# Performance work log

Measured on AMD Instinct MI355X. Metric: run time of the kernel, lower is better.

The kernel has to match this reference:

```python
import jax, jax.numpy as jnp
import numpy as np

EPS = 1e-06
NUM_HEADS = 8


def phi(x):
    # elu(x) + 1, a positive feature map
    return jax.nn.elu(x) + 1.0


def setup_inputs() -> dict:
    key = jax.random.key(0)
    ks = jax.random.split(key, 7)
    B, N, E = 4, 1024, 512
    s = 1.0 / np.sqrt(E)
    return {
        "Q": jax.random.normal(ks[0], (B, N, E), jnp.float32),
        "K": jax.random.normal(ks[1], (B, N, E), jnp.float32),
        "V": jax.random.normal(ks[2], (B, N, E), jnp.float32),
        "Wq": jax.random.normal(ks[3], (E, E), jnp.float32) * s,
        "Wk": jax.random.normal(ks[4], (E, E), jnp.float32) * s,
        "Wv": jax.random.normal(ks[5], (E, E), jnp.float32) * s,
        "Wo": jax.random.normal(ks[6], (E, E), jnp.float32) * s,
        "causal": 1,
    }


def _split_heads(x, H):
    B, N, E = x.shape
    return x.reshape(B, N, H, E // H).transpose(0, 2, 1, 3)  # (B,H,N,D)


def reference(Q, K, V, Wq, Wk, Wv, Wo, causal):
    B, N, E = Q.shape
    H = NUM_HEADS
    D = E // H
    # nn.Linear: y = x @ W.T (bias=False)
    Qf = phi(_split_heads(Q @ Wq.T, H))  # (B,H,N,D)
    Kf = phi(_split_heads(K @ Wk.T, H))  # (B,H,N,D)
    Vh = _split_heads(V @ Wv.T, H)       # (B,H,N,D)

    if causal:
        # prefix sums of outer products K_f V^T -> (B,H,N,D,Dv)
        KV_prefix = jnp.cumsum(Kf[..., :, None] * Vh[..., None, :], axis=2)
        Kf_prefix = jnp.cumsum(Kf, axis=2)
        num = jnp.einsum('bhnd,bhnde->bhne', Qf, KV_prefix)
        den = jnp.einsum('bhnd,bhnd->bhn', Qf, Kf_prefix)[..., None]
        out = num / (den + EPS)
    else:
        KV = jnp.einsum('bhnd,bhne->bhde', Kf, Vh)          # (B,H,D,Dv)
        Kf_sum = Kf.sum(axis=2)                              # (B,H,D)
        num = jnp.einsum('bhnd,bhde->bhne', Qf, KV)
        den = jnp.einsum('bhnd,bhd->bhn', Qf, Kf_sum)[..., None]
        out = num / (den + EPS)

    out = out.transpose(0, 2, 1, 3).reshape(B, N, E)
    return out @ Wo.T
```

## Files before the change

### kernel.cpp

```cpp
#include <hip/hip_runtime.h>
#include <stdint.h>

typedef __bf16 bf16;
typedef __attribute__((ext_vector_type(8))) __bf16 bfx8;
typedef __attribute__((ext_vector_type(4))) float f32x4;

__device__ inline f32x4 mfma16(bfx8 a, bfx8 b, f32x4 c) {
  return __builtin_amdgcn_mfma_f32_16x16x32_bf16(a, b, c, 0, 0, 0);
}

struct GemmArgs {
  const void* A[3];
  const void* Bt[3];
  bf16* ob[3];
  float* of;
  int phi_upto;
};

template <bool AF32, bool BF32, bool OUTF>
__global__ __launch_bounds__(256) void gemm_bt(GemmArgs ga) {
  const int z = blockIdx.z;
  const void* Ag = ga.A[z];
  const void* Bg = ga.Bt[z];
  const int tm = blockIdx.x * 128, tn = blockIdx.y * 128;
  const int tid = threadIdx.x, l = tid & 63, w = tid >> 6;
  const int wm = w >> 1, wn = w & 1, lm = l & 15, lk = l >> 4;

  __shared__ __align__(16) bf16 As[128 * 64];
  __shared__ __align__(16) bf16 Bs[128 * 64];

  f32x4 acc[4][4] = {};

  for (int kt = 0; kt < 8; ++kt) {
#pragma unroll
    for (int it = 0; it < 4; ++it) {
      int c = (it * 4 + w) * 64 + l;
      int row = c >> 3, t8 = c & 7;
      bfx8 v;
      if (AF32) {
        const float* s = (const float*)Ag + (size_t)(tm + row) * 512 + kt * 64 + t8 * 8;
        f32x4 x0 = *(const f32x4*)s;
        f32x4 x1 = *(const f32x4*)(s + 4);
        v[0] = (bf16)x0[0]; v[1] = (bf16)x0[1]; v[2] = (bf16)x0[2]; v[3] = (bf16)x0[3];
        v[4] = (bf16)x1[0]; v[5] = (bf16)x1[1]; v[6] = (bf16)x1[2]; v[7] = (bf16)x1[3];
      } else {
        v = *(const bfx8*)((const bf16*)Ag + (size_t)(tm + row) * 512 + kt * 64 + t8 * 8);
      }
      *(bfx8*)&As[row * 64 + ((t8 ^ (row & 7)) << 3)] = v;
    }
#pragma unroll
    for (int it = 0; it < 4; ++it) {
      int c = (it * 4 + w) * 64 + l;
      int row = c >> 3, t8 = c & 7;
      bfx8 v;
      if (BF32) {
        const float* s = (const float*)Bg + (size_t)(tn + row) * 512 + kt * 64 + t8 * 8;
        f32x4 x0 = *(const f32x4*)s;
        f32x4 x1 = *(const f32x4*)(s + 4);
        v[0] = (bf16)x0[0]; v[1] = (bf16)x0[1]; v[2] = (bf16)x0[2]; v[3] = (bf16)x0[3];
        v[4] = (bf16)x1[0]; v[5] = (bf16)x1[1]; v[6] = (bf16)x1[2]; v[7] = (bf16)x1[3];
      } else {
        v = *(const bfx8*)((const bf16*)Bg + (size_t)(tn + row) * 512 + kt * 64 + t8 * 8);
      }
      *(bfx8*)&Bs[row * 64 + ((t8 ^ (row & 7)) << 3)] = v;
    }
    __syncthreads();
#pragma unroll
    for (int ks = 0; ks < 2; ++ks) {
      bfx8 af[4], bfr[4];
#pragma unroll
      for (int i = 0; i < 4; ++i) {
        int ra = wm * 64 + i * 16 + lm;
        af[i] = *(const bfx8*)&As[ra * 64 + (((ks * 4 + lk) ^ (ra & 7)) << 3)];
        int rb = wn * 64 + i * 16 + lm;
        bfr[i] = *(const bfx8*)&Bs[rb * 64 + (((ks * 4 + lk) ^ (rb & 7)) << 3)];
      }
#pragma unroll
      for (int i = 0; i < 4; ++i)
#pragma unroll
        for (int j = 0; j < 4; ++j)
          acc[i][j] = mfma16(af[i], bfr[j], acc[i][j]);
    }
    __syncthreads();
  }

  const bool phi = z < ga.phi_upto;
#pragma unroll
  for (int i = 0; i < 4; ++i)
#pragma unroll
    for (int j = 0; j < 4; ++j)
#pragma unroll
      for (int r = 0; r < 4; ++r) {
        int m = tm + wm * 64 + i * 16 + lk * 4 + r;
        int n = tn + wn * 64 + j * 16 + lm;
        float v = acc[i][j][r];
        if (phi) v = v > 0.f ? v + 1.f : __expf(v);
        if (OUTF) ga.of[(size_t)m * 512 + n] = v;
        else ga.ob[z][(size_t)m * 512 + n] = (bf16)v;
      }
}

__global__ __launch_bounds__(256) void chunk_kv(const bf16* __restrict__ Kf,
                                                const bf16* __restrict__ Vh,
                                                float* __restrict__ KVs,
                                                float* __restrict__ ksums) {
  const int bh = blockIdx.x, c = blockIdx.y, b = bh >> 3, h = bh & 7;
  const int tid = threadIdx.x, l = tid & 63, w = tid >> 6, lm = l & 15, lk = l >> 4;
  __shared__ __align__(16) bf16 KTs[64 * 64];
  __shared__ __align__(16) bf16 VTs[64 * 64];
  __shared__ float ksum_p[256];

  const size_t base = (size_t)(b * 1024) * 512 + h * 64;
  const int sr = tid >> 2, sp = tid & 3;
  {
    const size_t g = base + (size_t)(c * 64 + sr) * 512 + sp * 16;
    bfx8 k0 = *(const bfx8*)&Kf[g], k1 = *(const bfx8*)&Kf[g + 8];
    bfx8 v0 = *(const bfx8*)&Vh[g], v1 = *(const bfx8*)&Vh[g + 8];
#pragma unroll
    for (int q = 0; q < 8; ++q) {
      int d0 = sp * 16 + q, d1 = sp * 16 + 8 + q;
      KTs[d0 * 64 + (((sr >> 3) ^ (d0 & 7)) << 3) + (sr & 7)] = k0[q];
      KTs[d1 * 64 + (((sr >> 3) ^ (d1 & 7)) << 3) + (sr & 7)] = k1[q];
      VTs[d0 * 64 + (((sr >> 3) ^ (d0 & 7)) << 3) + (sr & 7)] = v0[q];
      VTs[d1 * 64 + (((sr >> 3) ^ (d1 & 7)) << 3) + (sr & 7)] = v1[q];
    }
  }
  __syncthreads();
  {
    int d = tid & 63, jp = tid >> 6;
    float s = 0.f;
#pragma unroll
    for (int q = 0; q < 16; ++q) {
      int j = jp * 16 + q;
      s += (float)KTs[d * 64 + (((j >> 3) ^ (d & 7)) << 3) + (j & 7)];
    }
    ksum_p[jp * 64 + d] = s;
  }
  f32x4 kacc[4] = {};
#pragma unroll
  for (int ks = 0; ks < 2; ++ks) {
    int r = w * 16 + lm;
    bfx8 av = *(const bfx8*)&VTs[r * 64 + (((ks * 4 + lk) ^ (r & 7)) << 3)];
#pragma unroll
    for (int bn = 0; bn < 4; ++bn) {
      int e = bn * 16 + lm;
      bfx8 bk = *(const bfx8*)&KTs[e * 64 + (((ks * 4 + lk) ^ (e & 7)) << 3)];
      kacc[bn] = mfma16(av, bk, kacc[bn]);
    }
  }
  float* st = KVs + (size_t)(bh * 16 + c) * 4096;
#pragma unroll
  for (int bn = 0; bn < 4; ++bn)
#pragma unroll
    for (int rg = 0; rg < 4; ++rg) {
      int e = w * 16 + lk * 4 + rg, d = bn * 16 + lm;
      st[e * 64 + d] = kacc[bn][rg];
    }
  __syncthreads();
  if (tid < 64)
    ksums[(size_t)(bh * 16 + c) * 64 + tid] =
        ksum_p[tid] + ksum_p[64 + tid] + ksum_p[128 + tid] + ksum_p[192 + tid];
}

__global__ __launch_bounds__(256) void scan_kv(float* __restrict__ KVs,
                                               float* __restrict__ ksums) {
  const int bh = blockIdx.x, slice = blockIdx.y;
  const int tid = threadIdx.x;
  float* p = KVs + (size_t)bh * 16 * 4096 + slice * 256 + tid;
  float run = 0.f;
#pragma unroll
  for (int c = 0; c < 16; ++c) {
    float t = p[(size_t)c * 4096];
    p[(size_t)c * 4096] = run;
    run += t;
  }
  if (slice == 0 && tid < 64) {
    float* kp = ksums + (size_t)bh * 16 * 64 + tid;
    float rk = 0.f;
#pragma unroll
    for (int c = 0; c < 16; ++c) {
      float t = kp[(size_t)c * 64];
      kp[(size_t)c * 64] = rk;
      rk += t;
    }
  }
}

__global__ __launch_bounds__(256) void chunk_out(const bf16* __restrict__ Qf,
                                                 const bf16* __restrict__ Kf,
                                                 const bf16* __restrict__ Vh,
                                                 const float* __restrict__ KVs,
                                                 const float* __restrict__ ksums,
                                                 bf16* __restrict__ Ob) {
  const int bh = blockIdx.x, c = blockIdx.y, b = bh >> 3, h = bh & 7;
  const int tid = threadIdx.x, l = tid & 63, w = tid >> 6, lm = l & 15, lk = l >> 4;

  __shared__ __align__(16) bf16 Qs[64 * 64];
  __shared__ __align__(16) bf16 Ks[64 * 64];
  __shared__ __align__(16) bf16 VTs[64 * 64];
  __shared__ __align__(16) bf16 Ss[64 * 64];
  __shared__ float ksum[64], den_i[64], den_all[64], den_p[256];

  const size_t base = (size_t)(b * 1024) * 512 + h * 64;
  const int sr = tid >> 2, sp = tid & 3;
  {
    const size_t g = base + (size_t)(c * 64 + sr) * 512 + sp * 16;
    bfx8 q0 = *(const bfx8*)&Qf[g], q1 = *(const bfx8*)&Qf[g + 8];
    bfx8 k0 = *(const bfx8*)&Kf[g], k1 = *(const bfx8*)&Kf[g + 8];
    bfx8 v0 = *(const bfx8*)&Vh[g], v1 = *(const bfx8*)&Vh[g + 8];
    *(bfx8*)&Qs[sr * 64 + (((2 * sp) ^ (sr & 7)) << 3)] = q0;
    *(bfx8*)&Qs[sr * 64 + (((2 * sp + 1) ^ (sr & 7)) << 3)] = q1;
    *(bfx8*)&Ks[sr * 64 + (((2 * sp) ^ (sr & 7)) << 3)] = k0;
    *(bfx8*)&Ks[sr * 64 + (((2 * sp + 1) ^ (sr & 7)) << 3)] = k1;
#pragma unroll
    for (int q = 0; q < 8; ++q) {
      int d0 = sp * 16 + q, d1 = sp * 16 + 8 + q;
      VTs[d0 * 64 + (((sr >> 3) ^ (d0 & 7)) << 3) + (sr & 7)] = v0[q];
      VTs[d1 * 64 + (((sr >> 3) ^ (d1 & 7)) << 3) + (sr & 7)] = v1[q];
    }
  }
  if (tid < 64) ksum[tid] = ksums[(size_t)(bh * 16 + c) * 64 + tid];
  __syncthreads();

  f32x4 sacc[4] = {};
  bfx8 aq[2];
#pragma unroll
  for (int ks = 0; ks < 2; ++ks) {
    int r = w * 16 + lm;
    aq[ks] = *(const bfx8*)&Qs[r * 64 + (((ks * 4 + lk) ^ (r & 7)) << 3)];
#pragma unroll
    for (int bn = 0; bn < 4; ++bn) {
      int rb = bn * 16 + lm;
      bfx8 bk = *(const bfx8*)&Ks[rb * 64 + (((ks * 4 + lk) ^ (rb & 7)) << 3)];
      sacc[bn] = mfma16(aq[ks], bk, sacc[bn]);
    }
  }
  float prs[4] = {0.f, 0.f, 0.f, 0.f};
#pragma unroll
  for (int bn = 0; bn < 4; ++bn)
#pragma unroll
    for (int rg = 0; rg < 4; ++rg) {
      int i = w * 16 + lk * 4 + rg, j = bn * 16 + lm;
      float v = (j <= i) ? sacc[bn][rg] : 0.f;
      prs[rg] += v;
      Ss[i * 64 + (((j >> 3) ^ (i & 7)) << 3) + (j & 7)] = (bf16)v;
    }
#pragma unroll
  for (int m = 1; m < 16; m <<= 1) {
#pragma unroll
    for (int rg = 0; rg < 4; ++rg) prs[rg] += __shfl_xor(prs[rg], m, 64);
  }
  if (lm == 0) {
#pragma unroll
    for (int rg = 0; rg < 4; ++rg) den_i[w * 16 + lk * 4 + rg] = prs[rg];
  }
  {
    float s = 0.f;
#pragma unroll
    for (int q = 0; q < 16; ++q) {
      int d = sp * 16 + q;
      s += (float)Qs[sr * 64 + (((d >> 3) ^ (sr & 7)) << 3) + (d & 7)] * ksum[d];
    }
    den_p[sp * 64 + sr] = s;
  }
  __syncthreads();

  if (tid < 64)
    den_all[tid] = den_i[tid] + den_p[tid] + den_p[64 + tid] + den_p[128 + tid] + den_p[192 + tid];
  f32x4 oacc[4] = {};
  const float* st = KVs + (size_t)(bh * 16 + c) * 4096;
#pragma unroll
  for (int ks = 0; ks < 2; ++ks) {
    int r = w * 16 + lm;
    bfx8 as_ = *(const bfx8*)&Ss[r * 64 + (((ks * 4 + lk) ^ (r & 7)) << 3)];
#pragma unroll
    for (int bn = 0; bn < 4; ++bn) {
      int e = bn * 16 + lm;
      bfx8 bv = *(const bfx8*)&VTs[e * 64 + (((ks * 4 + lk) ^ (e & 7)) << 3)];
      oacc[bn] = mfma16(as_, bv, oacc[bn]);
      int d0 = ks * 32 + lk * 8;
      f32x4 x0 = *(const f32x4*)&st[e * 64 + d0];
      f32x4 x1 = *(const f32x4*)&st[e * 64 + d0 + 4];
      bfx8 bkv;
      bkv[0] = (bf16)x0[0]; bkv[1] = (bf16)x0[1]; bkv[2] = (bf16)x0[2]; bkv[3] = (bf16)x0[3];
      bkv[4] = (bf16)x1[0]; bkv[5] = (bf16)x1[1]; bkv[6] = (bf16)x1[2]; bkv[7] = (bf16)x1[3];
      oacc[bn] = mfma16(aq[ks], bkv, oacc[bn]);
    }
  }
  __syncthreads();

#pragma unroll
  for (int bn = 0; bn < 4; ++bn)
#pragma unroll
    for (int rg = 0; rg < 4; ++rg) {
      int i = w * 16 + lk * 4 + rg, e = bn * 16 + lm;
      float o = oacc[bn][rg] / (den_all[i] + 1e-6f);
      Ob[base + (size_t)(c * 64 + i) * 512 + e] = (bf16)o;
    }
}

extern "C" void kernel_launch(void* const* d_in, const int* in_sizes, int n_in,
                              void* d_out, int out_size, void* d_ws, size_t ws_size,
                              hipStream_t stream) {
  const float* Q = (const float*)d_in[0];
  const float* K = (const float*)d_in[1];
  const float* V = (const float*)d_in[2];
  const float* Wq = (const float*)d_in[3];
  const float* Wk = (const float*)d_in[4];
  const float* Wv = (const float*)d_in[5];
  const float* Wo = (const float*)d_in[6];
  (void)in_sizes; (void)n_in; (void)out_size; (void)ws_size;

  char* wsp = (char*)d_ws;
  const size_t MB = 1ull << 20;
  bf16* Qp = (bf16*)(wsp + 0 * MB);
  bf16* Kp = (bf16*)(wsp + 4 * MB);
  bf16* Vp = (bf16*)(wsp + 8 * MB);
  bf16* Ob = (bf16*)(wsp + 12 * MB);
  float* KVs = (float*)(wsp + 16 * MB);
  float* ksums = (float*)(wsp + 24 * MB);

  GemmArgs g1;
  g1.A[0] = Q;  g1.A[1] = K;  g1.A[2] = V;
  g1.Bt[0] = Wq; g1.Bt[1] = Wk; g1.Bt[2] = Wv;
  g1.ob[0] = Qp; g1.ob[1] = Kp; g1.ob[2] = Vp;
  g1.of = nullptr;
  g1.phi_upto = 2;
  gemm_bt<true, true, false><<<dim3(32, 4, 3), 256, 0, stream>>>(g1);

  chunk_kv<<<dim3(32, 16), 256, 0, stream>>>(Kp, Vp, KVs, ksums);
  scan_kv<<<dim3(32, 16), 256, 0, stream>>>(KVs, ksums);
  chunk_out<<<dim3(32, 16), 256, 0, stream>>>(Qp, Kp, Vp, KVs, ksums, Ob);

  GemmArgs g2;
  g2.A[0] = Ob; g2.A[1] = nullptr; g2.A[2] = nullptr;
  g2.Bt[0] = Wo; g2.Bt[1] = nullptr; g2.Bt[2] = nullptr;
  g2.ob[0] = nullptr; g2.ob[1] = nullptr; g2.ob[2] = nullptr;
  g2.of = (float*)d_out;
  g2.phi_upto = 0;
  gemm_bt<false, true, true><<<dim3(32, 4, 1), 256, 0, stream>>>(g2);
}
```

Baseline: 54.14 us.

## Fuse KV prefix scan into chunk_out, store chunk KV in bf16, halve GEMM M-tile

Removes the separate scan_kv launch. Each chunk_out block now sums the bf16 per-chunk KV states and the key sums of all preceding chunks itself and stages the result in shared memory. Per-chunk KV states are stored in bf16 instead of fp32, which halves their traffic but loses precision in the accumulation. The GEMM tile shrinks from 128x128 to 64x128, doubling the block count to improve occupancy on the many-CU device. Later chunks do redundant work that grows linearly with chunk index, which creates load imbalance.

```diff
diff --git a/kernel.cpp b/kernel.cpp
--- a/kernel.cpp
+++ b/kernel.cpp
@@ -22,19 +22,19 @@
   const int z = blockIdx.z;
   const void* Ag = ga.A[z];
   const void* Bg = ga.Bt[z];
-  const int tm = blockIdx.x * 128, tn = blockIdx.y * 128;
+  const int tm = blockIdx.x * 64, tn = blockIdx.y * 128;
   const int tid = threadIdx.x, l = tid & 63, w = tid >> 6;
   const int wm = w >> 1, wn = w & 1, lm = l & 15, lk = l >> 4;
 
-  __shared__ __align__(16) bf16 As[128 * 64];
+  __shared__ __align__(16) bf16 As[64 * 64];
   __shared__ __align__(16) bf16 Bs[128 * 64];
 
-  f32x4 acc[4][4] = {};
+  f32x4 acc[2][4] = {};
 
   for (int kt = 0; kt < 8; ++kt) {
 #pragma unroll
-    for (int it = 0; it < 4; ++it) {
-      int c = (it * 4 + w) * 64 + l;
+    for (int it = 0; it < 2; ++it) {
+      int c = it * 256 + tid;
       int row = c >> 3, t8 = c & 7;
       bfx8 v;
       if (AF32) {
@@ -50,7 +50,7 @@
     }
 #pragma unroll
     for (int it = 0; it < 4; ++it) {
-      int c = (it * 4 + w) * 64 + l;
+      int c = it * 256 + tid;
       int row = c >> 3, t8 = c & 7;
       bfx8 v;
       if (BF32) {
@@ -67,16 +67,19 @@
     __syncthreads();
 #pragma unroll
     for (int ks = 0; ks < 2; ++ks) {
-      bfx8 af[4], bfr[4];
-#pragma unroll
-      for (int i = 0; i < 4; ++i) {
-        int ra = wm * 64 + i * 16 + lm;
+      bfx8 af[2], bfr[4];
+#pragma unroll
+      for (int i = 0; i < 2; ++i) {
+        int ra = wm * 32 + i * 16 + lm;
         af[i] = *(const bfx8*)&As[ra * 64 + (((ks * 4 + lk) ^ (ra & 7)) << 3)];
-        int rb = wn * 64 + i * 16 + lm;
-        bfr[i] = *(const bfx8*)&Bs[rb * 64 + (((ks * 4 + lk) ^ (rb & 7)) << 3)];
-      }
-#pragma unroll
-      for (int i = 0; i < 4; ++i)
+      }
+#pragma unroll
+      for (int j = 0; j < 4; ++j) {
+        int rb = wn * 64 + j * 16 + lm;
+        bfr[j] = *(const bfx8*)&Bs[rb * 64 + (((ks * 4 + lk) ^ (rb & 7)) << 3)];
+      }
+#pragma unroll
+      for (int i = 0; i < 2; ++i)
 #pragma unroll
         for (int j = 0; j < 4; ++j)
           acc[i][j] = mfma16(af[i], bfr[j], acc[i][j]);
@@ -86,12 +89,12 @@
 
   const bool phi = z < ga.phi_upto;
 #pragma unroll
-  for (int i = 0; i < 4; ++i)
+  for (int i = 0; i < 2; ++i)
 #pragma unroll
     for (int j = 0; j < 4; ++j)
 #pragma unroll
       for (int r = 0; r < 4; ++r) {
-        int m = tm + wm * 64 + i * 16 + lk * 4 + r;
+        int m = tm + wm * 32 + i * 16 + lk * 4 + r;
         int n = tn + wn * 64 + j * 16 + lm;
         float v = acc[i][j][r];
         if (phi) v = v > 0.f ? v + 1.f : __expf(v);
@@ -102,7 +105,7 @@
 
 __global__ __launch_bounds__(256) void chunk_kv(const bf16* __restrict__ Kf,
                                                 const bf16* __restrict__ Vh,
-                                                float* __restrict__ KVs,
+                                                bf16* __restrict__ KVb,
                                                 float* __restrict__ ksums) {
   const int bh = blockIdx.x, c = blockIdx.y, b = bh >> 3, h = bh & 7;
   const int tid = threadIdx.x, l = tid & 63, w = tid >> 6, lm = l & 15, lk = l >> 4;
@@ -148,13 +151,13 @@
       kacc[bn] = mfma16(av, bk, kacc[bn]);
     }
   }
-  float* st = KVs + (size_t)(bh * 16 + c) * 4096;
+  bf16* st = KVb + (size_t)(bh * 16 + c) * 4096;
 #pragma unroll
   for (int bn = 0; bn < 4; ++bn)
 #pragma unroll
     for (int rg = 0; rg < 4; ++rg) {
       int e = w * 16 + lk * 4 + rg, d = bn * 16 + lm;
-      st[e * 64 + d] = kacc[bn][rg];
+      st[e * 64 + d] = (bf16)kacc[bn][rg];
     }
   __syncthreads();
   if (tid < 64)
@@ -162,34 +165,10 @@
         ksum_p[tid] + ksum_p[64 + tid] + ksum_p[128 + tid] + ksum_p[192 + tid];
 }
 
-__global__ __launch_bounds__(256) void scan_kv(float* __restrict__ KVs,
-                                               float* __restrict__ ksums) {
-  const int bh = blockIdx.x, slice = blockIdx.y;
-  const int tid = threadIdx.x;
-  float* p = KVs + (size_t)bh * 16 * 4096 + slice * 256 + tid;
-  float run = 0.f;
-#pragma unroll
-  for (int c = 0; c < 16; ++c) {
-    float t = p[(size_t)c * 4096];
-    p[(size_t)c * 4096] = run;
-    run += t;
-  }
-  if (slice == 0 && tid < 64) {
-    float* kp = ksums + (size_t)bh * 16 * 64 + tid;
-    float rk = 0.f;
-#pragma unroll
-    for (int c = 0; c < 16; ++c) {
-      float t = kp[(size_t)c * 64];
-      kp[(size_t)c * 64] = rk;
-      rk += t;
-    }
-  }
-}
-
 __global__ __launch_bounds__(256) void chunk_out(const bf16* __restrict__ Qf,
                                                  const bf16* __restrict__ Kf,
                                                  const bf16* __restrict__ Vh,
-                                                 const float* __restrict__ KVs,
+                                                 const bf16* __restrict__ KVb,
                                                  const float* __restrict__ ksums,
                                                  bf16* __restrict__ Ob) {
   const int bh = blockIdx.x, c = blockIdx.y, b = bh >> 3, h = bh & 7;
@@ -199,6 +178,7 @@
   __shared__ __align__(16) bf16 Ks[64 * 64];
   __shared__ __align__(16) bf16 VTs[64 * 64];
   __shared__ __align__(16) bf16 Ss[64 * 64];
+  __shared__ __align__(16) bf16 KVL[64 * 64];
   __shared__ float ksum[64], den_i[64], den_all[64], den_p[256];
 
   const size_t base = (size_t)(b * 1024) * 512 + h * 64;
@@ -219,7 +199,28 @@
       VTs[d1 * 64 + (((sr >> 3) ^ (d1 & 7)) << 3) + (sr & 7)] = v1[q];
     }
   }
-  if (tid < 64) ksum[tid] = ksums[(size_t)(bh * 16 + c) * 64 + tid];
+  {
+    const int e = sr, dp = sp * 16;
+    float s0[8] = {}, s1[8] = {};
+    const bf16* kb = KVb + (size_t)(bh * 16) * 4096 + e * 64 + dp;
+    for (int cc = 0; cc < c; ++cc) {
+      bfx8 x0 = *(const bfx8*)(kb + (size_t)cc * 4096);
+      bfx8 x1 = *(const bfx8*)(kb + (size_t)cc * 4096 + 8);
+#pragma unroll
+      for (int q = 0; q < 8; ++q) { s0[q] += (float)x0[q]; s1[q] += (float)x1[q]; }
+    }
+    bfx8 y0, y1;
+#pragma unroll
+    for (int q = 0; q < 8; ++q) { y0[q] = (bf16)s0[q]; y1[q] = (bf16)s1[q]; }
+    *(bfx8*)&KVL[e * 64 + (((2 * sp) ^ (e & 7)) << 3)] = y0;
+    *(bfx8*)&KVL[e * 64 + (((2 * sp + 1) ^ (e & 7)) << 3)] = y1;
+    if (tid < 64) {
+      float s = 0.f;
+      const float* kp = ksums + (size_t)(bh * 16) * 64 + tid;
+      for (int cc = 0; cc < c; ++cc) s += kp[(size_t)cc * 64];
+      ksum[tid] = s;
+    }
+  }
   __syncthreads();
 
   f32x4 sacc[4] = {};
@@ -268,7 +269,6 @@
   if (tid < 64)
     den_all[tid] = den_i[tid] + den_p[tid] + den_p[64 + tid] + den_p[128 + tid] + den_p[192 + tid];
   f32x4 oacc[4] = {};
-  const float* st = KVs + (size_t)(bh * 16 + c) * 4096;
 #pragma unroll
   for (int ks = 0; ks < 2; ++ks) {
     int r = w * 16 + lm;
@@ -278,12 +278,7 @@
       int e = bn * 16 + lm;
       bfx8 bv = *(const bfx8*)&VTs[e * 64 + (((ks * 4 + lk) ^ (e & 7)) << 3)];
       oacc[bn] = mfma16(as_, bv, oacc[bn]);
-      int d0 = ks * 32 + lk * 8;
-      f32x4 x0 = *(const f32x4*)&st[e * 64 + d0];
-      f32x4 x1 = *(const f32x4*)&st[e * 64 + d0 + 4];
-      bfx8 bkv;
-      bkv[0] = (bf16)x0[0]; bkv[1] = (bf16)x0[1]; bkv[2] = (bf16)x0[2]; bkv[3] = (bf16)x0[3];
-      bkv[4] = (bf16)x1[0]; bkv[5] = (bf16)x1[1]; bkv[6] = (bf16)x1[2]; bkv[7] = (bf16)x1[3];
+      bfx8 bkv = *(const bfx8*)&KVL[e * 64 + (((ks * 4 + lk) ^ (e & 7)) << 3)];
       oacc[bn] = mfma16(aq[ks], bkv, oacc[bn]);
     }
   }
@@ -317,7 +312,7 @@
   bf16* Kp = (bf16*)(wsp + 4 * MB);
   bf16* Vp = (bf16*)(wsp + 8 * MB);
   bf16* Ob = (bf16*)(wsp + 12 * MB);
-  float* KVs = (float*)(wsp + 16 * MB);
+  bf16* KVb = (bf16*)(wsp + 16 * MB);
   float* ksums = (float*)(wsp + 24 * MB);
 
   GemmArgs g1;
@@ -326,11 +321,10 @@
   g1.ob[0] = Qp; g1.ob[1] = Kp; g1.ob[2] = Vp;
   g1.of = nullptr;
   g1.phi_upto = 2;
-  gemm_bt<true, true, false><<<dim3(32, 4, 3), 256, 0, stream>>>(g1);
-
-  chunk_kv<<<dim3(32, 16), 256, 0, stream>>>(Kp, Vp, KVs, ksums);
-  scan_kv<<<dim3(32, 16), 256, 0, stream>>>(KVs, ksums);
-  chunk_out<<<dim3(32, 16), 256, 0, stream>>>(Qp, Kp, Vp, KVs, ksums, Ob);
+  gemm_bt<true, true, false><<<dim3(64, 4, 3), 256, 0, stream>>>(g1);
+
+  chunk_kv<<<dim3(32, 16), 256, 0, stream>>>(Kp, Vp, KVb, ksums);
+  chunk_out<<<dim3(32, 16), 256, 0, stream>>>(Qp, Kp, Vp, KVb, ksums, Ob);
 
   GemmArgs g2;
   g2.A[0] = Ob; g2.A[1] = nullptr; g2.A[2] = nullptr;
@@ -338,5 +332,5 @@
   g2.ob[0] = nullptr; g2.ob[1] = nullptr; g2.ob[2] = nullptr;
   g2.of = (float*)d_out;
   g2.phi_upto = 0;
-  gemm_bt<false, true, true><<<dim3(32, 4, 1), 256, 0, stream>>>(g2);
-}
+  gemm_bt<false, true, true><<<dim3(64, 4, 1), 256, 0, stream>>>(g2);
+}
```

Result: no change. 54.20 us (+0.1%).
